# Performance work log

Hardware: AMD Instinct MI355X
Metric: run time of the kernel (lower is better)

The kernel has to match this reference:

```python
import jax, jax.numpy as jnp
import numpy as np

L_IN, L_FREQ, L_OUT = 128, 64, 64
C_IN, C_OUT, T_DIM = 64, 64, 256
SPIN = 1

# ---------- self-contained spin-weighted SHT (MW sampling), replacing s2fft ----------

def _mw_thetas(L, extended):
    n = 2 * L - 1 if extended else L
    return (2 * np.arange(n) + 1) * np.pi / (2 * L - 1)

def _wigner_d_stack(L, thetas, n):
    # d^l_{m,n}(theta) = <l,m| exp(-i theta Jy) |l,n>, computed via eigh of the
    # Hermitian angular-momentum operator Jy. Output (ntheta, L, 2L-1), m at col L-1+m.
    nth = len(thetas)
    out = np.zeros((nth, L, 2 * L - 1), dtype=np.float64)
    for l in range(abs(n), L):
        dim = 2 * l + 1
        m = np.arange(-l, l).astype(np.float64)
        ap = np.sqrt(l * (l + 1.0) - m * (m + 1.0))
        Jy = np.zeros((dim, dim), dtype=np.complex128)
        i = np.arange(dim - 1)
        Jy[i + 1, i] = -0.5j * ap
        Jy[i, i + 1] = 0.5j * ap
        lam, V = np.linalg.eigh(Jy)
        coeff = V * np.conj(V[l + n, :])[None, :]
        phases = np.exp(-1j * np.outer(lam, thetas))
        out[:, l, L - 1 - l:L + l] = (coeff @ phases).T.real
    return out

def _mw_quad_weights(L):
    # per-theta weights on the mirror-extended grid: q_t = (1/(2L-1)) sum_k w(k) e^{ik theta_t}
    # with w(k) = int_0^pi e^{ik t} sin(t) dt
    k = np.arange(-(L - 1), L)
    den = np.where(np.abs(k) == 1, 1, 1 - k * k).astype(np.float64)
    w = np.where(k % 2 == 0, 2.0 / den, 0.0).astype(np.complex128)
    w[k == 1] = 0.5j * np.pi
    w[k == -1] = -0.5j * np.pi
    th = _mw_thetas(L, True)
    return ((w[None, :] * np.exp(1j * np.outer(th, k))).sum(1) / (2 * L - 1)).real

# transform kernels are constants (built once at import, numpy)
_D_FWD = jnp.asarray(_wigner_d_stack(L_IN, _mw_thetas(L_IN, True), -SPIN) * _mw_quad_weights(L_IN)[:, None, None], jnp.float32)
_D_INV = jnp.asarray(_wigner_d_stack(L_OUT, _mw_thetas(L_OUT, False), -SPIN), jnp.float32)
_CL_IN = jnp.asarray(((-1.0) ** SPIN) * np.sqrt((2 * np.arange(L_IN) + 1) / (4 * np.pi)), jnp.float32)
_CL_OUT = jnp.asarray(((-1.0) ** SPIN) * np.sqrt((2 * np.arange(L_OUT) + 1) / (4 * np.pi)), jnp.float32)
_m_all = np.arange(-(L_IN - 1), L_IN)
_PARITY = jnp.asarray(np.where((_m_all + SPIN) % 2 == 0, 1.0, -1.0), jnp.float32)

def sht_forward(x):
    # x: (L_IN, 2*L_IN-1, C) real spatial -> flm: (L_IN, 2*L_IN-1, C) complex, m at L_IN-1+m
    nphi = 2 * L_IN - 1
    ftm = jnp.fft.fftshift(jnp.fft.fft(x, axis=1), axes=1) * (2 * jnp.pi / nphi)
    # mirror extension in theta with (-1)^(m+spin) parity (all channels at once)
    g_ext = jnp.concatenate([ftm, _PARITY[None, :, None] * ftm[::-1][1:]], axis=0)
    flm = jnp.einsum('tlm,tmc->lmc', _D_FWD, g_ext)
    return flm * _CL_IN[:, None, None]

def sht_inverse(flm):
    # flm: (L_OUT, 2*L_OUT-1, C) complex -> (L_OUT, 2*L_OUT-1, C) real spatial
    ftm = jnp.einsum('tlm,lmc->tmc', _D_INV, flm * _CL_OUT[:, None, None])
    return (jnp.fft.ifft(jnp.fft.ifftshift(ftm, axes=1), axis=1) * (2 * L_OUT - 1)).real

def resize_flm(flm, l_in, l_out):
    # centered truncation / zero-pad of (L, 2L-1, C) harmonic coefficients
    if l_out <= l_in:
        d = l_in - l_out
        return flm[:l_out, d:d + 2 * l_out - 1]
    d = l_out - l_in
    return jnp.pad(flm, ((0, d), (d, d), (0, 0)))

# ---------- inputs and parameters ----------

def setup_inputs():
    key = jax.random.key(0)
    ks = jax.random.split(key, 12)
    n = lambda i, shape, s: jax.random.normal(ks[i], shape, jnp.float32) * s
    return {
        'x': jax.random.normal(ks[0], (L_IN, 2 * L_IN - 1, C_IN), jnp.float32),
        't_emb': jax.random.normal(ks[1], (T_DIM,), jnp.float32),
        'spec_conv_w': n(2, (C_IN, C_OUT), (1.0 / C_IN) ** 0.5),
        'spec_conv_b': jnp.zeros((C_OUT,), jnp.float32),
        'spec_wr': n(3, (L_FREQ, C_IN, C_OUT), (0.5 / C_IN) ** 0.5),
        'spec_wi': n(4, (L_FREQ, C_IN, C_OUT), (0.5 / C_IN) ** 0.5),
        'spec_tr_w': n(5, (T_DIM, L_FREQ), (1.0 / T_DIM) ** 0.5),
        'spec_tr_b': jnp.zeros((L_FREQ,), jnp.float32),
        'spec_ti_w': n(6, (T_DIM, L_FREQ), (1.0 / T_DIM) ** 0.5),
        'spec_ti_b': jnp.zeros((L_FREQ,), jnp.float32),
        'spat_conv1_w': n(7, (C_IN, C_OUT), (1.0 / C_IN) ** 0.5),
        'spat_conv1_b': jnp.zeros((C_OUT,), jnp.float32),
        'spat_t_w': n(8, (T_DIM, 2 * C_OUT), (1.0 / T_DIM) ** 0.5),
        'spat_t_b': jnp.zeros((2 * C_OUT,), jnp.float32),
        'spat_weight': n(9, (C_OUT, C_OUT), 0.01),
        'spat_conv2_w': n(10, (C_OUT, C_OUT), (1.0 / C_OUT) ** 0.5),
        'spat_conv2_b': jnp.zeros((C_OUT,), jnp.float32),
        'ln_scale': jnp.ones((C_OUT,), jnp.float32),
        'ln_bias': jnp.zeros((C_OUT,), jnp.float32),
    }

def reference(x, t_emb, spec_conv_w, spec_conv_b, spec_wr, spec_wi, spec_tr_w, spec_tr_b, spec_ti_w, spec_ti_b, spat_conv1_w, spat_conv1_b, spat_t_w, spat_t_b, spat_weight, spat_conv2_w, spat_conv2_b, ln_scale, ln_bias):
    # ----- SphericalSpectralTimeConv branch -----
    flm = sht_forward(x)                                   # (L_IN, 2L_IN-1, C_IN) complex
    flm = resize_flm(flm, L_IN, L_FREQ)                    # (L_FREQ, 2L_FREQ-1, C_IN)
    conv_flm = jnp.einsum('lmi,io->lmo', flm, spec_conv_w) + spec_conv_b
    t_c = (t_emb @ spec_tr_w + spec_tr_b) + 1j * (t_emb @ spec_ti_w + spec_ti_b)   # (L_FREQ,)
    w = t_c[:, None, None] * (spec_wr + 1j * spec_wi)      # (L_FREQ, C_IN, C_OUT)
    flm = jnp.einsum('lmi,lio->lmo', flm, w) + conv_flm
    xs = sht_inverse(resize_flm(flm, L_FREQ, L_OUT))       # (L_OUT, 2L_OUT-1, C_OUT) real
    xs = xs / (jnp.linalg.norm(xs, axis=-1, keepdims=True) + 1e-6)
    # ----- SpatialTimeConv branch (path='down') -----
    h = jnp.einsum('lmi,io->lmo', x, spat_conv1_w) + spat_conv1_b
    t = t_emb @ spat_t_w + spat_t_b
    w_t, b_t = t[:C_OUT], t[C_OUT:]
    h = jnp.einsum('lmi,io->lmo', h, w_t[None, :] * spat_weight)
    h = sht_inverse(resize_flm(sht_forward(h), L_IN, L_OUT))
    h = jnp.einsum('lmi,io->lmo', h, spat_conv2_w) + spat_conv2_b + b_t
    # ----- combine: add, gelu, LayerNorm (eps=1e-6 over channels) -----
    y = jax.nn.gelu(xs + h)
    mu = jnp.mean(y, axis=-1, keepdims=True)
    var = jnp.var(y, axis=-1, keepdims=True)
    return (y - mu) * jax.lax.rsqrt(var + 1e-6) * ln_scale + ln_bias
```

## Files before the change

### kernel.cpp

```cpp
#include <hip/hip_runtime.h>
#include <math.h>

#define DPI 3.141592653589793238462643383279502884

__device__ __forceinline__ float wave_sum64(float v) {
#pragma unroll
  for (int off = 32; off > 0; off >>= 1) v += __shfl_xor(v, off, 64);
  return v;
}

__device__ __forceinline__ float gelu_tanh(float v) {
  float u = 0.7978845608028654f * (v + 0.044715f * v * v * v);
  return 0.5f * v * (1.0f + tanhf(u));
}

#define CN255F ((float)(-2.0 * DPI / 255.0))
#define CN127F ((float)(2.0 * DPI / 127.0))

__global__ __launch_bounds__(256) void ct_setup(
    float* __restrict__ Deff, float* __restrict__ Dinv,
    const float* __restrict__ temb, const float* __restrict__ trw,
    const float* __restrict__ trb, const float* __restrict__ tiw,
    const float* __restrict__ tib, const float* __restrict__ stw,
    const float* __restrict__ stb, const float* __restrict__ scw,
    const float* __restrict__ swr, const float* __restrict__ swi,
    const float* __restrict__ c1w, const float* __restrict__ c1b,
    const float* __restrict__ sweight,
    float2* __restrict__ A2, float* __restrict__ Mm,
    float* __restrict__ bias2, float* __restrict__ tv) {
  __shared__ double red[64];
  __shared__ float clf[64];
  __shared__ float fb1[256];
  __shared__ float fb2[256];
  int b = blockIdx.x;
  int tid = threadIdx.x;
  if (b >= 255) {
    if (b < 319) {
      int l = b - 255;
      fb1[tid] = temb[tid] * trw[tid * 64 + l];
      fb2[tid] = temb[tid] * tiw[tid * 64 + l];
      __syncthreads();
      for (int s = 128; s > 0; s >>= 1) {
        if (tid < s) { fb1[tid] += fb1[tid + s]; fb2[tid] += fb2[tid + s]; }
        __syncthreads();
      }
      float tr = fb1[0] + trb[l], ti = fb2[0] + tib[l];
      int o = tid & 63, iq = tid >> 6;
      for (int i = iq * 16; i < iq * 16 + 16; ++i) {
        int idx = (l * 64 + i) * 64 + o;
        float r = swr[idx], s2 = swi[idx];
        A2[idx] = make_float2(scw[i * 64 + o] + tr * r - ti * s2, tr * s2 + ti * r);
      }
    } else if (b < 383) {
      int j = b - 319;
      int o = tid & 63, part = tid >> 6;
      float p = 0.f;
      for (int k = part * 64; k < part * 64 + 64; ++k)
        p = fmaf(temb[k], stw[k * 128 + o], p);
      fb1[part * 64 + o] = p;
      __syncthreads();
      if (part == 0) fb2[o] = fb1[o] + fb1[64 + o] + fb1[128 + o] + fb1[192 + o] + stb[o];
      __syncthreads();
      float tvo = fb2[o];
      float q = 0.f;
      for (int i = part * 16; i < part * 16 + 16; ++i)
        q = fmaf(c1w[j * 64 + i], sweight[i * 64 + o], q);
      __syncthreads();
      fb1[part * 64 + o] = q;
      __syncthreads();
      if (part == 0) Mm[j * 64 + o] = tvo * (fb1[o] + fb1[64 + o] + fb1[128 + o] + fb1[192 + o]);
      if (j == 0) {
        float bq = 0.f;
        for (int i = part * 16; i < part * 16 + 16; ++i)
          bq = fmaf(c1b[i], sweight[i * 64 + o], bq);
        __syncthreads();
        fb1[part * 64 + o] = bq;
        __syncthreads();
        if (part == 0) bias2[o] = tvo * (fb1[o] + fb1[64 + o] + fb1[128 + o] + fb1[192 + o]);
      }
    } else {
      int o = tid & 127, part = tid >> 7;
      float p = 0.f;
      for (int k = part * 128; k < part * 128 + 128; ++k)
        p = fmaf(temb[k], stw[k * 128 + o], p);
      fb1[part * 128 + o] = p;
      __syncthreads();
      if (part == 0) tv[o] = fb1[o] + fb1[128 + o] + stb[o];
    }
    return;
  }
  int mode = (b < 128) ? 0 : 1;
  if (tid < 64) clf[tid] = (float)(-sqrt((2.0 * tid + 1.0) / (4.0 * DPI)));
  int t, mm;
  if (mode == 0) { t = b; mm = tid; }
  else { mm = b - 128; t = tid; }
  double denomN = (mode == 0) ? 255.0 : 127.0;
  double beta = (2.0 * t + 1.0) * DPI / denomN;
  float coeff;
  if (mode == 0) {
    if (tid < 63) {
      int k = 2 * (tid + 1);
      red[tid] = 8.0 * cos((double)k * beta) / (1.0 - (double)k * (double)k);
    } else if (tid == 63) {
      red[63] = 4.0;
    }
    __syncthreads();
    for (int s = 32; s > 0; s >>= 1) {
      if (tid < s) red[tid] += red[tid + s];
      __syncthreads();
    }
    double s = red[0] / 255.0;
    if (t == 127) s *= 0.5;
    coeff = (float)(s * (2.0 * DPI / 255.0));
    if (tid >= 127) return;
  } else {
    __syncthreads();
    coeff = 1.0f;
    if (tid >= 64) return;
  }
  int m = mm - 63;
  double cb = cos(beta);
  double ch = cos(0.5 * beta), sh = sin(0.5 * beta);
  int am = (m < 0) ? -m : m;
  int l0v = (am > 1) ? am : 1;
  double seed;
  if (m >= 1) {
    double j = (double)m;
    double K = exp(0.5 * (lgamma(2.0 * j + 1.0) - lgamma(j) - lgamma(j + 2.0)));
    double sgn = ((m + 1) & 1) ? -1.0 : 1.0;
    seed = sgn * K * pow(ch, j - 1.0) * pow(sh, j + 1.0);
  } else if (m <= -1) {
    double j = (double)(-m);
    double K = exp(0.5 * (lgamma(2.0 * j + 1.0) - lgamma(j) - lgamma(j + 2.0)));
    seed = K * pow(ch, j + 1.0) * pow(sh, j - 1.0);
  } else {
    seed = -sqrt(2.0) * sh * ch;
  }
  float dl = (float)seed, dm1 = 0.0f, S_cur = 0.0f;
  float cbf = (float)cb, mf = (float)m;
  for (int l = 0; l < 64; ++l) {
    float val = 0.0f;
    if (l >= l0v) {
      val = dl * coeff * clf[l];
      float Ld = (float)l, lp = Ld + 1.0f;
      float S_next = sqrtf((lp * lp - mf * mf) * (lp * lp - 1.0f));
      float num1 = (2.0f * Ld + 1.0f) * (Ld * lp * cbf + mf);
      float dn = (num1 * dl - lp * S_cur * dm1) / (Ld * S_next);
      dm1 = dl; dl = dn; S_cur = S_next;
    }
    if (mode == 0) Deff[((size_t)t * 127 + mm) * 64 + l] = val;
    else Dinv[((size_t)mm * 64 + l) * 64 + t] = val;
  }
}

__global__ __launch_bounds__(256) void ct_dft(const float* __restrict__ x,
                                              float* __restrict__ Are, float* __restrict__ Aim,
                                              float* __restrict__ Bre, float* __restrict__ Bim) {
  __shared__ float xs_[64][64];
  __shared__ float tsr[64][64], tsi[64][64];
  int t = blockIdx.x, mh = blockIdx.y, ph = blockIdx.z;
  float* ore = ph ? Bre : Are;
  float* oim = ph ? Bim : Aim;
  int pbase = ph * 128;
  int Ktot = ph ? 127 : 128;
  int tid = threadIdx.x;
  int cg_ = tid & 15, mg = tid >> 4;
  float accr[4][4], acci[4][4];
#pragma unroll
  for (int j = 0; j < 4; ++j)
#pragma unroll
    for (int q = 0; q < 4; ++q) { accr[j][q] = 0.f; acci[j][q] = 0.f; }
  for (int k0 = 0; k0 < Ktot; k0 += 64) {
    int kn = (Ktot - k0 < 64) ? Ktot - k0 : 64;
    __syncthreads();
    {
      int r = tid >> 2, c4 = (tid & 3) * 16;
      if (r < kn) {
        const float4* src = (const float4*)(x + ((size_t)t * 255 + pbase + k0 + r) * 64 + c4);
        float4* dst = (float4*)&xs_[r][c4];
        dst[0] = src[0]; dst[1] = src[1]; dst[2] = src[2]; dst[3] = src[3];
      }
    }
    for (int e = tid; e < 64 * 64; e += 256) {
      int r = e >> 6, mi = e & 63;
      if (r < kn) {
        int gcol = mh * 64 + mi; if (gcol > 126) gcol = 126;
        int p = pbase + k0 + r;
        float ang = CN255F * (float)((gcol - 63) * p);
        float sv, cv;
        __sincosf(ang, &sv, &cv);
        tsr[r][mi] = cv; tsi[r][mi] = sv;
      }
    }
    __syncthreads();
#pragma unroll 4
    for (int k = 0; k < kn; ++k) {
      float4 xv = *(const float4*)&xs_[k][cg_ * 4];
      float4 tr4 = *(const float4*)&tsr[k][mg * 4];
      float4 ti4 = *(const float4*)&tsi[k][mg * 4];
      float xv4[4] = {xv.x, xv.y, xv.z, xv.w};
      float trv[4] = {tr4.x, tr4.y, tr4.z, tr4.w};
      float tiv[4] = {ti4.x, ti4.y, ti4.z, ti4.w};
#pragma unroll
      for (int j = 0; j < 4; ++j)
#pragma unroll
        for (int q = 0; q < 4; ++q) {
          accr[j][q] = fmaf(xv4[q], trv[j], accr[j][q]);
          acci[j][q] = fmaf(xv4[q], tiv[j], acci[j][q]);
        }
    }
  }
#pragma unroll
  for (int j = 0; j < 4; ++j) {
    int gmm = mh * 64 + mg * 4 + j;
    if (gmm > 126) continue;
    size_t ob = ((size_t)t * 127 + gmm) * 64 + cg_ * 4;
    *(float4*)(ore + ob) = make_float4(accr[j][0], accr[j][1], accr[j][2], accr[j][3]);
    *(float4*)(oim + ob) = make_float4(acci[j][0], acci[j][1], acci[j][2], acci[j][3]);
  }
}

__global__ __launch_bounds__(256) void ct_projf(const float* __restrict__ Deff,
                                                const float* __restrict__ fAre,
                                                const float* __restrict__ fAim,
                                                const float* __restrict__ fBre,
                                                const float* __restrict__ fBim,
                                                float* __restrict__ flmA_re, float* __restrict__ flmA_im,
                                                float* __restrict__ flmB_re, float* __restrict__ flmB_im) {
  __shared__ float Dsh[64][32];
  __shared__ float fr_[64][64], fi_[64][64];
  int mm = blockIdx.x, lh = blockIdx.y, th = blockIdx.z;
  float* ore = th ? flmB_re : flmA_re;
  float* oim = th ? flmB_im : flmA_im;
  int tb = th * 64;
  int tid = threadIdx.x;
  int cg_ = tid & 15, lg = tid >> 4;
  for (int e = tid; e < 64 * 32; e += 256) {
    int r = e >> 5, li = e & 31;
    Dsh[r][li] = Deff[((size_t)(tb + r) * 127 + mm) * 64 + lh * 32 + li];
  }
  for (int e = tid; e < 64 * 64; e += 256) {
    int r = e >> 6, c = e & 63;
    size_t idx = ((size_t)(tb + r) * 127 + mm) * 64 + c;
    fr_[r][c] = fAre[idx] + fBre[idx];
    fi_[r][c] = fAim[idx] + fBim[idx];
  }
  __syncthreads();
  float ar[2][4], ai[2][4];
#pragma unroll
  for (int li = 0; li < 2; ++li)
#pragma unroll
    for (int q = 0; q < 4; ++q) { ar[li][q] = 0.f; ai[li][q] = 0.f; }
#pragma unroll 4
  for (int k = 0; k < 64; ++k) {
    float4 fr4 = *(const float4*)&fr_[k][cg_ * 4];
    float4 fi4 = *(const float4*)&fi_[k][cg_ * 4];
    float2 d2 = *(const float2*)&Dsh[k][lg * 2];
    float frv[4] = {fr4.x, fr4.y, fr4.z, fr4.w};
    float fiv[4] = {fi4.x, fi4.y, fi4.z, fi4.w};
    float dv[2] = {d2.x, d2.y};
#pragma unroll
    for (int li = 0; li < 2; ++li)
#pragma unroll
      for (int q = 0; q < 4; ++q) {
        ar[li][q] = fmaf(dv[li], frv[q], ar[li][q]);
        ai[li][q] = fmaf(dv[li], fiv[q], ai[li][q]);
      }
  }
#pragma unroll
  for (int li = 0; li < 2; ++li) {
    size_t row = ((size_t)mm * 64 + lh * 32 + lg * 2 + li) * 64 + cg_ * 4;
    *(float4*)(ore + row) = make_float4(ar[li][0], ar[li][1], ar[li][2], ar[li][3]);
    *(float4*)(oim + row) = make_float4(ai[li][0], ai[li][1], ai[li][2], ai[li][3]);
  }
}

__global__ __launch_bounds__(256) void ct_mix(const float* __restrict__ flmA_re,
                                              const float* __restrict__ flmA_im,
                                              const float* __restrict__ flmB_re,
                                              const float* __restrict__ flmB_im,
                                              const float2* __restrict__ A2,
                                              const float* __restrict__ Mm,
                                              const float* __restrict__ scb,
                                              const float* __restrict__ bias2,
                                              const float* __restrict__ Deff,
                                              float* __restrict__ s_re, float* __restrict__ s_im,
                                              float* __restrict__ h_re, float* __restrict__ h_im) {
  __shared__ float Ar_[64][32], Ai_[64][32], Msh[64][32];
  __shared__ float Br_[64][65], Bi_[64][65];
  __shared__ float rb[256];
  int l = blockIdx.x, mh = blockIdx.y, oh = blockIdx.z;
  int tid = threadIdx.x;
  int og = tid & 15, mg = tid >> 4;
  rb[tid] = (mh == 0 && tid < 128) ? Deff[((size_t)tid * 127 + 63) * 64 + l] : 0.f;
  __syncthreads();
  for (int s = 128; s > 0; s >>= 1) {
    if (tid < s) rb[tid] += rb[tid + s];
    __syncthreads();
  }
  float slv = rb[0];
  for (int e = tid; e < 64 * 32; e += 256) {
    int r = e >> 5, oi = e & 31;
    float2 aa = A2[((size_t)l * 64 + r) * 64 + oh * 32 + oi];
    Ar_[r][oi] = aa.x; Ai_[r][oi] = aa.y;
    Msh[r][oi] = Mm[r * 64 + oh * 32 + oi];
  }
  for (int e = tid; e < 64 * 64; e += 256) {
    int mi = e >> 6, i = e & 63;
    int gmm = mh * 64 + mi; if (gmm > 126) gmm = 126;
    size_t idx = ((size_t)gmm * 64 + l) * 64 + i;
    Br_[mi][i] = flmA_re[idx] + flmB_re[idx];
    Bi_[mi][i] = flmA_im[idx] + flmB_im[idx];
  }
  __syncthreads();
  int o0 = oh * 32 + og * 2;
  float b0[2] = {scb[o0], scb[o0 + 1]};
  float sr[4][2], si[4][2], hr[4][2], hi[4][2];
#pragma unroll
  for (int jm = 0; jm < 4; ++jm)
#pragma unroll
    for (int qo = 0; qo < 2; ++qo) {
      sr[jm][qo] = b0[qo]; si[jm][qo] = 0.f; hr[jm][qo] = 0.f; hi[jm][qo] = 0.f;
    }
#pragma unroll 4
  for (int k = 0; k < 64; ++k) {
    float2 ar2 = *(const float2*)&Ar_[k][og * 2];
    float2 ai2 = *(const float2*)&Ai_[k][og * 2];
    float2 mv2 = *(const float2*)&Msh[k][og * 2];
    float br4[4], bi4[4];
#pragma unroll
    for (int jm = 0; jm < 4; ++jm) {
      br4[jm] = Br_[mg * 4 + jm][k];
      bi4[jm] = Bi_[mg * 4 + jm][k];
    }
    float arv[2] = {ar2.x, ar2.y}, aiv[2] = {ai2.x, ai2.y}, mvv[2] = {mv2.x, mv2.y};
#pragma unroll
    for (int jm = 0; jm < 4; ++jm)
#pragma unroll
      for (int qo = 0; qo < 2; ++qo) {
        sr[jm][qo] = fmaf(br4[jm], arv[qo], sr[jm][qo]);
        sr[jm][qo] = fmaf(-bi4[jm], aiv[qo], sr[jm][qo]);
        si[jm][qo] = fmaf(br4[jm], aiv[qo], si[jm][qo]);
        si[jm][qo] = fmaf(bi4[jm], arv[qo], si[jm][qo]);
        hr[jm][qo] = fmaf(br4[jm], mvv[qo], hr[jm][qo]);
        hi[jm][qo] = fmaf(bi4[jm], mvv[qo], hi[jm][qo]);
      }
  }
  float bb[2] = {bias2[o0], bias2[o0 + 1]};
#pragma unroll
  for (int jm = 0; jm < 4; ++jm) {
    int gmm = mh * 64 + mg * 4 + jm;
    if (gmm > 126) continue;
    if (gmm == 63) {
#pragma unroll
      for (int qo = 0; qo < 2; ++qo)
        hr[jm][qo] = fmaf(255.0f * slv, bb[qo], hr[jm][qo]);
    }
    size_t row = ((size_t)gmm * 64 + l) * 64 + o0;
    *(float2*)(s_re + row) = make_float2(sr[jm][0], sr[jm][1]);
    *(float2*)(s_im + row) = make_float2(si[jm][0], si[jm][1]);
    *(float2*)(h_re + row) = make_float2(hr[jm][0], hr[jm][1]);
    *(float2*)(h_im + row) = make_float2(hi[jm][0], hi[jm][1]);
  }
}

__global__ __launch_bounds__(256) void ct_proji(const float* __restrict__ Dinv,
                                                const float* __restrict__ s_re,
                                                const float* __restrict__ s_im,
                                                const float* __restrict__ h_re,
                                                const float* __restrict__ h_im,
                                                float* __restrict__ fos_re, float* __restrict__ fos_im,
                                                float* __restrict__ foh_re, float* __restrict__ foh_im) {
  __shared__ float Dsh[64][64];
  __shared__ float Br_[64][32], Bi_[64][32];
  int mm = blockIdx.x, br = blockIdx.y, ch = blockIdx.z;
  const float* ire = br ? h_re : s_re;
  const float* iim = br ? h_im : s_im;
  float* ore = br ? foh_re : fos_re;
  float* oim = br ? foh_im : fos_im;
  int tid = threadIdx.x;
  int cg_ = tid & 15, tg = tid >> 4;
  for (int e = tid; e < 64 * 64; e += 256) {
    int r = e >> 6, tt = e & 63;
    Dsh[r][tt] = Dinv[((size_t)mm * 64 + r) * 64 + tt];
  }
  for (int e = tid; e < 64 * 32; e += 256) {
    int r = e >> 5, cc = e & 31;
    size_t idx = ((size_t)mm * 64 + r) * 64 + ch * 32 + cc;
    Br_[r][cc] = ire[idx];
    Bi_[r][cc] = iim[idx];
  }
  __syncthreads();
  float ar[4][2], ai[4][2];
#pragma unroll
  for (int j = 0; j < 4; ++j)
#pragma unroll
    for (int q = 0; q < 2; ++q) { ar[j][q] = 0.f; ai[j][q] = 0.f; }
#pragma unroll 4
  for (int k = 0; k < 64; ++k) {
    float4 d4 = *(const float4*)&Dsh[k][tg * 4];
    float2 fr2 = *(const float2*)&Br_[k][cg_ * 2];
    float2 fi2 = *(const float2*)&Bi_[k][cg_ * 2];
    float dv[4] = {d4.x, d4.y, d4.z, d4.w};
    float frv[2] = {fr2.x, fr2.y}, fiv[2] = {fi2.x, fi2.y};
#pragma unroll
    for (int j = 0; j < 4; ++j)
#pragma unroll
      for (int q = 0; q < 2; ++q) {
        ar[j][q] = fmaf(dv[j], frv[q], ar[j][q]);
        ai[j][q] = fmaf(dv[j], fiv[q], ai[j][q]);
      }
  }
#pragma unroll
  for (int j = 0; j < 4; ++j) {
    int t = tg * 4 + j;
    size_t ob = ((size_t)t * 127 + mm) * 64 + ch * 32 + cg_ * 2;
    *(float2*)(ore + ob) = make_float2(ar[j][0], ar[j][1]);
    *(float2*)(oim + ob) = make_float2(ai[j][0], ai[j][1]);
  }
}

__global__ __launch_bounds__(256) void ct_idft(const float* __restrict__ fos_re,
                                               const float* __restrict__ fos_im,
                                               const float* __restrict__ foh_re,
                                               const float* __restrict__ foh_im,
                                               float* __restrict__ xsbA, float* __restrict__ xsbB,
                                               float* __restrict__ hsbA, float* __restrict__ hsbB) {
  __shared__ float Ar_[32][64], Ai_[32][64], Br_[32][64], Bi_[32][64];
  int t = blockIdx.x, br = blockIdx.y;
  int z = blockIdx.z;
  int ph = z >> 1, kh = z & 1;
  const float* fre = br ? foh_re : fos_re;
  const float* fim = br ? foh_im : fos_im;
  float* outp = br ? (kh ? hsbB : hsbA) : (kh ? xsbB : xsbA);
  int kbase = kh * 64;
  int Ktot = kh ? 63 : 64;
  int tid = threadIdx.x;
  int cg_ = tid & 15, pg = tid >> 4;
  float acc[4][4];
#pragma unroll
  for (int j = 0; j < 4; ++j)
#pragma unroll
    for (int q = 0; q < 4; ++q) acc[j][q] = 0.f;
  for (int k0 = 0; k0 < Ktot; k0 += 32) {
    int kn = (Ktot - k0 < 32) ? Ktot - k0 : 32;
    __syncthreads();
    for (int e = tid; e < 32 * 64; e += 256) {
      int r = e >> 6, j = e & 63;
      if (r < kn) {
        int gmm = kbase + k0 + r;
        int gp = ph * 64 + j; if (gp > 126) gp = 126;
        float ang = CN127F * (float)((gmm - 63) * gp);
        float sv, cv;
        __sincosf(ang, &sv, &cv);
        Ar_[r][j] = cv; Ai_[r][j] = sv;
        size_t bidx = ((size_t)t * 127 + gmm) * 64 + j;
        Br_[r][j] = fre[bidx]; Bi_[r][j] = fim[bidx];
      }
    }
    __syncthreads();
#pragma unroll 4
    for (int k = 0; k < kn; ++k) {
      float4 a_r = *(const float4*)&Ar_[k][pg * 4];
      float4 a_i = *(const float4*)&Ai_[k][pg * 4];
      float4 b_r = *(const float4*)&Br_[k][cg_ * 4];
      float4 b_i = *(const float4*)&Bi_[k][cg_ * 4];
      float arv[4] = {a_r.x, a_r.y, a_r.z, a_r.w};
      float aiv[4] = {a_i.x, a_i.y, a_i.z, a_i.w};
      float brv[4] = {b_r.x, b_r.y, b_r.z, b_r.w};
      float biv[4] = {b_i.x, b_i.y, b_i.z, b_i.w};
#pragma unroll
      for (int j = 0; j < 4; ++j)
#pragma unroll
        for (int q = 0; q < 4; ++q) {
          acc[j][q] = fmaf(brv[q], arv[j], acc[j][q]);
          acc[j][q] = fmaf(biv[q], -aiv[j], acc[j][q]);
        }
    }
  }
#pragma unroll
  for (int j = 0; j < 4; ++j) {
    int gp = ph * 64 + pg * 4 + j;
    if (gp > 126) continue;
    *(float4*)(outp + ((size_t)t * 127 + gp) * 64 + cg_ * 4) =
        make_float4(acc[j][0], acc[j][1], acc[j][2], acc[j][3]);
  }
}

__global__ __launch_bounds__(256) void ct_fin(const float* __restrict__ xsbA,
                                              const float* __restrict__ xsbB,
                                              const float* __restrict__ hsbA,
                                              const float* __restrict__ hsbB,
                                              const float* __restrict__ c2w,
                                              const float* __restrict__ c2b,
                                              const float* __restrict__ tv,
                                              const float* __restrict__ lns,
                                              const float* __restrict__ lnb,
                                              float* __restrict__ out) {
  int w = threadIdx.x >> 6, lane = threadIdx.x & 63;
  size_t row = (size_t)blockIdx.x * 4 + w;
  size_t base = row * 64 + lane;
  float hv = hsbA[base] + hsbB[base];
  float xv = xsbA[base] + xsbB[base];
  float acc = c2b[lane] + tv[64 + lane];
#pragma unroll 16
  for (int i = 0; i < 64; ++i)
    acc = fmaf(__shfl(hv, i, 64), c2w[i * 64 + lane], acc);
  float ss = wave_sum64(xv * xv);
  xv = xv / (sqrtf(ss) + 1e-6f);
  float y = xv + acc;
  float g = gelu_tanh(y);
  float mu = wave_sum64(g) * (1.0f / 64.0f);
  float d = g - mu;
  float var = wave_sum64(d * d) * (1.0f / 64.0f);
  out[base] = d * rsqrtf(var + 1e-6f) * lns[lane] + lnb[lane];
}

extern "C" void kernel_launch(void* const* d_in, const int* in_sizes, int n_in,
                              void* d_out, int out_size, void* d_ws, size_t ws_size,
                              hipStream_t stream) {
  const float* x = (const float*)d_in[0];
  const float* temb = (const float*)d_in[1];
  const float* scw = (const float*)d_in[2];
  const float* scb = (const float*)d_in[3];
  const float* swr = (const float*)d_in[4];
  const float* swi = (const float*)d_in[5];
  const float* strw = (const float*)d_in[6];
  const float* strb = (const float*)d_in[7];
  const float* stiw = (const float*)d_in[8];
  const float* stib = (const float*)d_in[9];
  const float* c1w = (const float*)d_in[10];
  const float* c1b = (const float*)d_in[11];
  const float* stw = (const float*)d_in[12];
  const float* stb = (const float*)d_in[13];
  const float* sweight = (const float*)d_in[14];
  const float* c2w = (const float*)d_in[15];
  const float* c2b = (const float*)d_in[16];
  const float* lns = (const float*)d_in[17];
  const float* lnb = (const float*)d_in[18];
  float* out = (float*)d_out;

  char* base = (char*)d_ws;
  size_t off = 0;
  auto alloc = [&](size_t bytes) -> void* {
    void* p = base + off;
    off += (bytes + 255) & ~(size_t)255;
    return p;
  };
  float* tv = (float*)alloc(128 * sizeof(float));
  float* Mm = (float*)alloc(4096 * sizeof(float));
  float* bias2 = (float*)alloc(64 * sizeof(float));
  float2* A2 = (float2*)alloc(262144 * sizeof(float2));
  float* Deff = (float*)alloc(1040384 * sizeof(float));
  float* Dinv = (float*)alloc(520192 * sizeof(float));
  float* ftmA_re = (float*)alloc(1040384 * sizeof(float));
  float* ftmA_im = (float*)alloc(1040384 * sizeof(float));
  float* ftmB_re = (float*)alloc(1040384 * sizeof(float));
  float* ftmB_im = (float*)alloc(1040384 * sizeof(float));
  float* flmA_re = (float*)alloc(520192 * sizeof(float));
  float* flmA_im = (float*)alloc(520192 * sizeof(float));
  float* flmB_re = (float*)alloc(520192 * sizeof(float));
  float* flmB_im = (float*)alloc(520192 * sizeof(float));
  if (off > ws_size) return;
  float* s_re = ftmA_re;
  float* s_im = ftmA_im;
  float* h_re = ftmB_re;
  float* h_im = ftmB_im;
  float* fos_re = Deff;
  float* fos_im = Deff + 520192;
  float* foh_re = flmA_re;
  float* foh_im = flmA_im;
  float* xsbA = flmB_re;
  float* xsbB = flmB_im;
  float* hsbA = ftmA_re;
  float* hsbB = ftmA_im;

  hipLaunchKernelGGL(ct_setup, dim3(384), dim3(256), 0, stream, Deff, Dinv,
                     temb, strw, strb, stiw, stib, stw, stb,
                     scw, swr, swi, c1w, c1b, sweight, A2, Mm, bias2, tv);
  hipLaunchKernelGGL(ct_dft, dim3(128, 2, 2), dim3(256), 0, stream, x,
                     ftmA_re, ftmA_im, ftmB_re, ftmB_im);
  hipLaunchKernelGGL(ct_projf, dim3(127, 2, 2), dim3(256), 0, stream, Deff,
                     ftmA_re, ftmA_im, ftmB_re, ftmB_im,
                     flmA_re, flmA_im, flmB_re, flmB_im);
  hipLaunchKernelGGL(ct_mix, dim3(64, 2, 2), dim3(256), 0, stream,
                     flmA_re, flmA_im, flmB_re, flmB_im, A2, Mm, scb, bias2, Deff,
                     s_re, s_im, h_re, h_im);
  hipLaunchKernelGGL(ct_proji, dim3(127, 2, 2), dim3(256), 0, stream, Dinv,
                     s_re, s_im, h_re, h_im, fos_re, fos_im, foh_re, foh_im);
  hipLaunchKernelGGL(ct_idft, dim3(64, 2, 4), dim3(256), 0, stream,
                     fos_re, fos_im, foh_re, foh_im, xsbA, xsbB, hsbA, hsbB);
  hipLaunchKernelGGL(ct_fin, dim3(2032), dim3(256), 0, stream, xsbA, xsbB, hsbA, hsbB,
                     c2w, c2b, tv, lns, lnb, out);
}
```

Measured before the change: 211.9 us.

## Merge setup and DFT kernels into one launch, use float log-factorial seeds

Combines the former setup kernel (Wigner tables, time-embedding weights) and the DFT kernel into one heterogeneous kernel that dispatches on block index, so the independent work runs concurrently in a single launch. The Wigner seed computation swaps double-precision lgamma/pow for a float prefix-sum log-factorial table and __expf. Sharing one 48KB shared-memory buffer across roles may lower occupancy for the small setup blocks, and the float seeds add precision risk for large |m|.

```diff
diff --git a/kernel.cpp b/kernel.cpp
--- a/kernel.cpp
+++ b/kernel.cpp
@@ -17,86 +17,96 @@
 #define CN255F ((float)(-2.0 * DPI / 255.0))
 #define CN127F ((float)(2.0 * DPI / 127.0))
 
-__global__ __launch_bounds__(256) void ct_setup(
-    float* __restrict__ Deff, float* __restrict__ Dinv,
-    const float* __restrict__ temb, const float* __restrict__ trw,
-    const float* __restrict__ trb, const float* __restrict__ tiw,
-    const float* __restrict__ tib, const float* __restrict__ stw,
-    const float* __restrict__ stb, const float* __restrict__ scw,
-    const float* __restrict__ swr, const float* __restrict__ swi,
-    const float* __restrict__ c1w, const float* __restrict__ c1b,
-    const float* __restrict__ sweight,
-    float2* __restrict__ A2, float* __restrict__ Mm,
-    float* __restrict__ bias2, float* __restrict__ tv) {
-  __shared__ double red[64];
-  __shared__ float clf[64];
-  __shared__ float fb1[256];
-  __shared__ float fb2[256];
-  int b = blockIdx.x;
-  int tid = threadIdx.x;
-  if (b >= 255) {
-    if (b < 319) {
-      int l = b - 255;
-      fb1[tid] = temb[tid] * trw[tid * 64 + l];
-      fb2[tid] = temb[tid] * tiw[tid * 64 + l];
-      __syncthreads();
-      for (int s = 128; s > 0; s >>= 1) {
-        if (tid < s) { fb1[tid] += fb1[tid + s]; fb2[tid] += fb2[tid + s]; }
-        __syncthreads();
+
+__device__ __forceinline__ void dft_block(int idx, int tid, const float* __restrict__ x,
+                                          float* __restrict__ Are, float* __restrict__ Aim,
+                                          float* __restrict__ Bre, float* __restrict__ Bim,
+                                          char* sm) {
+  float* xs_ = (float*)sm;
+  float* tsr = (float*)(sm + 16384);
+  float* tsi = (float*)(sm + 32768);
+  int t = idx >> 2, mh = (idx >> 1) & 1, ph = idx & 1;
+  float* ore = ph ? Bre : Are;
+  float* oim = ph ? Bim : Aim;
+  int pbase = ph * 128;
+  int Ktot = ph ? 127 : 128;
+  int cg_ = tid & 15, mg = tid >> 4;
+  float accr[4][4], acci[4][4];
+#pragma unroll
+  for (int j = 0; j < 4; ++j)
+#pragma unroll
+    for (int q = 0; q < 4; ++q) { accr[j][q] = 0.f; acci[j][q] = 0.f; }
+  for (int k0 = 0; k0 < Ktot; k0 += 64) {
+    int kn = (Ktot - k0 < 64) ? Ktot - k0 : 64;
+    __syncthreads();
+    {
+      int r = tid >> 2, c4 = (tid & 3) * 16;
+      if (r < kn) {
+        const float4* src = (const float4*)(x + ((size_t)t * 255 + pbase + k0 + r) * 64 + c4);
+        float4* dst = (float4*)&xs_[r * 64 + c4];
+        dst[0] = src[0]; dst[1] = src[1]; dst[2] = src[2]; dst[3] = src[3];
       }
-      float tr = fb1[0] + trb[l], ti = fb2[0] + tib[l];
-      int o = tid & 63, iq = tid >> 6;
-      for (int i = iq * 16; i < iq * 16 + 16; ++i) {
-        int idx = (l * 64 + i) * 64 + o;
-        float r = swr[idx], s2 = swi[idx];
-        A2[idx] = make_float2(scw[i * 64 + o] + tr * r - ti * s2, tr * s2 + ti * r);
+    }
+    for (int e = tid; e < 64 * 64; e += 256) {
+      int r = e >> 6, mi = e & 63;
+      if (r < kn) {
+        int gcol = mh * 64 + mi; if (gcol > 126) gcol = 126;
+        int p = pbase + k0 + r;
+        float ang = CN255F * (float)((gcol - 63) * p);
+        float sv, cv;
+        __sincosf(ang, &sv, &cv);
+        tsr[r * 64 + mi] = cv; tsi[r * 64 + mi] = sv;
       }
-    } else if (b < 383) {
-      int j = b - 319;
-      int o = tid & 63, part = tid >> 6;
-      float p = 0.f;
-      for (int k = part * 64; k < part * 64 + 64; ++k)
-        p = fmaf(temb[k], stw[k * 128 + o], p);
-      fb1[part * 64 + o] = p;
-      __syncthreads();
-      if (part == 0) fb2[o] = fb1[o] + fb1[64 + o] + fb1[128 + o] + fb1[192 + o] + stb[o];
-      __syncthreads();
-      float tvo = fb2[o];
-      float q = 0.f;
-      for (int i = part * 16; i < part * 16 + 16; ++i)
-        q = fmaf(c1w[j * 64 + i], sweight[i * 64 + o], q);
-      __syncthreads();
-      fb1[part * 64 + o] = q;
-      __syncthreads();
-      if (part == 0) Mm[j * 64 + o] = tvo * (fb1[o] + fb1[64 + o] + fb1[128 + o] + fb1[192 + o]);
-      if (j == 0) {
-        float bq = 0.f;
-        for (int i = part * 16; i < part * 16 + 16; ++i)
-          bq = fmaf(c1b[i], sweight[i * 64 + o], bq);
-        __syncthreads();
-        fb1[part * 64 + o] = bq;
-        __syncthreads();
-        if (part == 0) bias2[o] = tvo * (fb1[o] + fb1[64 + o] + fb1[128 + o] + fb1[192 + o]);
-      }
-    } else {
-      int o = tid & 127, part = tid >> 7;
-      float p = 0.f;
-      for (int k = part * 128; k < part * 128 + 128; ++k)
-        p = fmaf(temb[k], stw[k * 128 + o], p);
-      fb1[part * 128 + o] = p;
-      __syncthreads();
-      if (part == 0) tv[o] = fb1[o] + fb1[128 + o] + stb[o];
-    }
-    return;
-  }
-  int mode = (b < 128) ? 0 : 1;
+    }
+    __syncthreads();
+#pragma unroll 4
+    for (int k = 0; k < kn; ++k) {
+      float4 xv = *(const float4*)&xs_[k * 64 + cg_ * 4];
+      float4 tr4 = *(const float4*)&tsr[k * 64 + mg * 4];
+      float4 ti4 = *(const float4*)&tsi[k * 64 + mg * 4];
+      float xv4[4] = {xv.x, xv.y, xv.z, xv.w};
+      float trv[4] = {tr4.x, tr4.y, tr4.z, tr4.w};
+      float tiv[4] = {ti4.x, ti4.y, ti4.z, ti4.w};
+#pragma unroll
+      for (int j = 0; j < 4; ++j)
+#pragma unroll
+        for (int q = 0; q < 4; ++q) {
+          accr[j][q] = fmaf(xv4[q], trv[j], accr[j][q]);
+          acci[j][q] = fmaf(xv4[q], tiv[j], acci[j][q]);
+        }
+    }
+  }
+#pragma unroll
+  for (int j = 0; j < 4; ++j) {
+    int gmm = mh * 64 + mg * 4 + j;
+    if (gmm > 126) continue;
+    size_t ob = ((size_t)t * 127 + gmm) * 64 + cg_ * 4;
+    *(float4*)(ore + ob) = make_float4(accr[j][0], accr[j][1], accr[j][2], accr[j][3]);
+    *(float4*)(oim + ob) = make_float4(acci[j][0], acci[j][1], acci[j][2], acci[j][3]);
+  }
+}
+
+__device__ __forceinline__ void wigner_block(int wb, int tid, float* __restrict__ Deff,
+                                             float* __restrict__ Dinv, char* sm) {
+  float* LF = (float*)sm;
+  double* red = (double*)(sm + 512);
+  float* clf = (float*)(sm + 1024);
+  int mode = (wb < 128) ? 0 : 1;
+  int t, mm;
+  if (mode == 0) { t = wb; mm = tid; }
+  else { mm = wb - 128; t = (tid < 64) ? tid : 63; }
   if (tid < 64) clf[tid] = (float)(-sqrt((2.0 * tid + 1.0) / (4.0 * DPI)));
-  int t, mm;
-  if (mode == 0) { t = b; mm = tid; }
-  else { mm = b - 128; t = tid; }
+  if (tid < 128) LF[tid] = (tid == 0) ? 0.f : logf((float)tid);
+  __syncthreads();
+  for (int s = 1; s < 128; s <<= 1) {
+    float add = (tid < 128 && tid >= s) ? LF[tid - s] : 0.f;
+    __syncthreads();
+    if (tid < 128) LF[tid] += add;
+    __syncthreads();
+  }
   double denomN = (mode == 0) ? 255.0 : 127.0;
   double beta = (2.0 * t + 1.0) * DPI / denomN;
-  float coeff;
+  float coeff = 1.0f;
   if (mode == 0) {
     if (tid < 63) {
       int k = 2 * (tid + 1);
@@ -112,32 +122,30 @@
     double s = red[0] / 255.0;
     if (t == 127) s *= 0.5;
     coeff = (float)(s * (2.0 * DPI / 255.0));
-    if (tid >= 127) return;
-  } else {
-    __syncthreads();
-    coeff = 1.0f;
-    if (tid >= 64) return;
-  }
+  }
+  bool active = (mode == 0) ? (tid < 127) : (tid < 64);
+  if (!active) return;
   int m = mm - 63;
-  double cb = cos(beta);
-  double ch = cos(0.5 * beta), sh = sin(0.5 * beta);
+  double chd, shd;
+  sincos(0.5 * beta, &shd, &chd);
+  float cbf = (float)cos(beta);
+  float chf = (float)chd, shf = (float)shd;
   int am = (m < 0) ? -m : m;
   int l0v = (am > 1) ? am : 1;
-  double seed;
-  if (m >= 1) {
-    double j = (double)m;
-    double K = exp(0.5 * (lgamma(2.0 * j + 1.0) - lgamma(j) - lgamma(j + 2.0)));
-    double sgn = ((m + 1) & 1) ? -1.0 : 1.0;
-    seed = sgn * K * pow(ch, j - 1.0) * pow(sh, j + 1.0);
-  } else if (m <= -1) {
-    double j = (double)(-m);
-    double K = exp(0.5 * (lgamma(2.0 * j + 1.0) - lgamma(j) - lgamma(j + 2.0)));
-    seed = K * pow(ch, j + 1.0) * pow(sh, j - 1.0);
+  float seed;
+  if (m == 0) {
+    seed = -1.4142135623730951f * shf * chf;
   } else {
-    seed = -sqrt(2.0) * sh * ch;
-  }
-  float dl = (float)seed, dm1 = 0.0f, S_cur = 0.0f;
-  float cbf = (float)cb, mf = (float)m;
+    int j = am;
+    float lch = logf(chf), lsh = logf(shf);
+    float e0 = 0.5f * (LF[2 * j] - LF[j - 1] - LF[j + 1]);
+    float expo = (m >= 1) ? e0 + (float)(j - 1) * lch + (float)(j + 1) * lsh
+                          : e0 + (float)(j + 1) * lch + (float)(j - 1) * lsh;
+    float sv = __expf(expo);
+    seed = (m >= 1 && ((m + 1) & 1)) ? -sv : sv;
+  }
+  float dl = seed, dm1 = 0.0f, S_cur = 0.0f;
+  float mf = (float)m;
   for (int l = 0; l < 64; ++l) {
     float val = 0.0f;
     if (l >= l0v) {
@@ -153,71 +161,98 @@
   }
 }
 
-__global__ __launch_bounds__(256) void ct_dft(const float* __restrict__ x,
-                                              float* __restrict__ Are, float* __restrict__ Aim,
-                                              float* __restrict__ Bre, float* __restrict__ Bim) {
-  __shared__ float xs_[64][64];
-  __shared__ float tsr[64][64], tsi[64][64];
-  int t = blockIdx.x, mh = blockIdx.y, ph = blockIdx.z;
-  float* ore = ph ? Bre : Are;
-  float* oim = ph ? Bim : Aim;
-  int pbase = ph * 128;
-  int Ktot = ph ? 127 : 128;
+__device__ __forceinline__ void a2_block(int l, int tid, const float* __restrict__ temb,
+                                         const float* __restrict__ trw, const float* __restrict__ trb,
+                                         const float* __restrict__ tiw, const float* __restrict__ tib,
+                                         const float* __restrict__ scw, const float* __restrict__ swr,
+                                         const float* __restrict__ swi, float2* __restrict__ A2,
+                                         char* sm) {
+  float* fb1 = (float*)sm;
+  float* fb2 = (float*)(sm + 1024);
+  fb1[tid] = temb[tid] * trw[tid * 64 + l];
+  fb2[tid] = temb[tid] * tiw[tid * 64 + l];
+  __syncthreads();
+  for (int s = 128; s > 0; s >>= 1) {
+    if (tid < s) { fb1[tid] += fb1[tid + s]; fb2[tid] += fb2[tid + s]; }
+    __syncthreads();
+  }
+  float tr = fb1[0] + trb[l], ti = fb2[0] + tib[l];
+  int o = tid & 63, iq = tid >> 6;
+  for (int i = iq * 16; i < iq * 16 + 16; ++i) {
+    int idx = (l * 64 + i) * 64 + o;
+    float r = swr[idx], s2 = swi[idx];
+    A2[idx] = make_float2(scw[i * 64 + o] + tr * r - ti * s2, tr * s2 + ti * r);
+  }
+}
+
+__device__ __forceinline__ void m_block(int j, int tid, const float* __restrict__ temb,
+                                        const float* __restrict__ stw, const float* __restrict__ stb,
+                                        const float* __restrict__ c1w, const float* __restrict__ c1b,
+                                        const float* __restrict__ sweight, float* __restrict__ Mm,
+                                        float* __restrict__ bias2, char* sm) {
+  float* fb1 = (float*)sm;
+  float* fb2 = (float*)(sm + 1024);
+  int o = tid & 63, part = tid >> 6;
+  float p = 0.f;
+  for (int k = part * 64; k < part * 64 + 64; ++k)
+    p = fmaf(temb[k], stw[k * 128 + o], p);
+  fb1[part * 64 + o] = p;
+  __syncthreads();
+  if (part == 0) fb2[o] = fb1[o] + fb1[64 + o] + fb1[128 + o] + fb1[192 + o] + stb[o];
+  __syncthreads();
+  float tvo = fb2[o];
+  float q = 0.f;
+  for (int i = part * 16; i < part * 16 + 16; ++i)
+    q = fmaf(c1w[j * 64 + i], sweight[i * 64 + o], q);
+  __syncthreads();
+  fb1[part * 64 + o] = q;
+  __syncthreads();
+  if (part == 0) Mm[j * 64 + o] = tvo * (fb1[o] + fb1[64 + o] + fb1[128 + o] + fb1[192 + o]);
+  if (j == 0) {
+    float bq = 0.f;
+    for (int i = part * 16; i < part * 16 + 16; ++i)
+      bq = fmaf(c1b[i], sweight[i * 64 + o], bq);
+    __syncthreads();
+    fb1[part * 64 + o] = bq;
+    __syncthreads();
+    if (part == 0) bias2[o] = tvo * (fb1[o] + fb1[64 + o] + fb1[128 + o] + fb1[192 + o]);
+  }
+}
+
+__device__ __forceinline__ void tv_block(int tid, const float* __restrict__ temb,
+                                         const float* __restrict__ stw, const float* __restrict__ stb,
+                                         float* __restrict__ tv, char* sm) {
+  float* fb1 = (float*)sm;
+  int o = tid & 127, part = tid >> 7;
+  float p = 0.f;
+  for (int k = part * 128; k < part * 128 + 128; ++k)
+    p = fmaf(temb[k], stw[k * 128 + o], p);
+  fb1[part * 128 + o] = p;
+  __syncthreads();
+  if (part == 0) tv[o] = fb1[o] + fb1[128 + o] + stb[o];
+}
+
+__global__ __launch_bounds__(256) void ct_pre(
+    const float* __restrict__ x, const float* __restrict__ temb,
+    const float* __restrict__ trw, const float* __restrict__ trb,
+    const float* __restrict__ tiw, const float* __restrict__ tib,
+    const float* __restrict__ stw, const float* __restrict__ stb,
+    const float* __restrict__ scw, const float* __restrict__ swr,
+    const float* __restrict__ swi, const float* __restrict__ c1w,
+    const float* __restrict__ c1b, const float* __restrict__ sweight,
+    float* __restrict__ Deff, float* __restrict__ Dinv,
+    float2* __restrict__ A2, float* __restrict__ Mm,
+    float* __restrict__ bias2, float* __restrict__ tv,
+    float* __restrict__ ftmA_re, float* __restrict__ ftmA_im,
+    float* __restrict__ ftmB_re, float* __restrict__ ftmB_im) {
+  __shared__ __align__(16) char sm[49152];
+  int vb = blockIdx.x;
   int tid = threadIdx.x;
-  int cg_ = tid & 15, mg = tid >> 4;
-  float accr[4][4], acci[4][4];
-#pragma unroll
-  for (int j = 0; j < 4; ++j)
-#pragma unroll
-    for (int q = 0; q < 4; ++q) { accr[j][q] = 0.f; acci[j][q] = 0.f; }
-  for (int k0 = 0; k0 < Ktot; k0 += 64) {
-    int kn = (Ktot - k0 < 64) ? Ktot - k0 : 64;
-    __syncthreads();
-    {
-      int r = tid >> 2, c4 = (tid & 3) * 16;
-      if (r < kn) {
-        const float4* src = (const float4*)(x + ((size_t)t * 255 + pbase + k0 + r) * 64 + c4);
-        float4* dst = (float4*)&xs_[r][c4];
-        dst[0] = src[0]; dst[1] = src[1]; dst[2] = src[2]; dst[3] = src[3];
-      }
-    }
-    for (int e = tid; e < 64 * 64; e += 256) {
-      int r = e >> 6, mi = e & 63;
-      if (r < kn) {
-        int gcol = mh * 64 + mi; if (gcol > 126) gcol = 126;
-        int p = pbase + k0 + r;
-        float ang = CN255F * (float)((gcol - 63) * p);
-        float sv, cv;
-        __sincosf(ang, &sv, &cv);
-        tsr[r][mi] = cv; tsi[r][mi] = sv;
-      }
-    }
-    __syncthreads();
-#pragma unroll 4
-    for (int k = 0; k < kn; ++k) {
-      float4 xv = *(const float4*)&xs_[k][cg_ * 4];
-      float4 tr4 = *(const float4*)&tsr[k][mg * 4];
-      float4 ti4 = *(const float4*)&tsi[k][mg * 4];
-      float xv4[4] = {xv.x, xv.y, xv.z, xv.w};
-      float trv[4] = {tr4.x, tr4.y, tr4.z, tr4.w};
-      float tiv[4] = {ti4.x, ti4.y, ti4.z, ti4.w};
-#pragma unroll
-      for (int j = 0; j < 4; ++j)
-#pragma unroll
-        for (int q = 0; q < 4; ++q) {
-          accr[j][q] = fmaf(xv4[q], trv[j], accr[j][q]);
-          acci[j][q] = fmaf(xv4[q], tiv[j], acci[j][q]);
-        }
-    }
-  }
-#pragma unroll
-  for (int j = 0; j < 4; ++j) {
-    int gmm = mh * 64 + mg * 4 + j;
-    if (gmm > 126) continue;
-    size_t ob = ((size_t)t * 127 + gmm) * 64 + cg_ * 4;
-    *(float4*)(ore + ob) = make_float4(accr[j][0], accr[j][1], accr[j][2], accr[j][3]);
-    *(float4*)(oim + ob) = make_float4(acci[j][0], acci[j][1], acci[j][2], acci[j][3]);
-  }
+  if (vb < 512) dft_block(vb, tid, x, ftmA_re, ftmA_im, ftmB_re, ftmB_im, sm);
+  else if (vb < 767) wigner_block(vb - 512, tid, Deff, Dinv, sm);
+  else if (vb < 831) a2_block(vb - 767, tid, temb, trw, trb, tiw, tib, scw, swr, swi, A2, sm);
+  else if (vb < 895) m_block(vb - 831, tid, temb, stw, stb, c1w, c1b, sweight, Mm, bias2, sm);
+  else tv_block(tid, temb, stw, stb, tv, sm);
 }
 
 __global__ __launch_bounds__(256) void ct_projf(const float* __restrict__ Deff,
@@ -575,10 +610,10 @@
   float* hsbA = ftmA_re;
   float* hsbB = ftmA_im;
 
-  hipLaunchKernelGGL(ct_setup, dim3(384), dim3(256), 0, stream, Deff, Dinv,
-                     temb, strw, strb, stiw, stib, stw, stb,
-                     scw, swr, swi, c1w, c1b, sweight, A2, Mm, bias2, tv);
-  hipLaunchKernelGGL(ct_dft, dim3(128, 2, 2), dim3(256), 0, stream, x,
+  hipLaunchKernelGGL(ct_pre, dim3(896), dim3(256), 0, stream,
+                     x, temb, strw, strb, stiw, stib, stw, stb,
+                     scw, swr, swi, c1w, c1b, sweight,
+                     Deff, Dinv, A2, Mm, bias2, tv,
                      ftmA_re, ftmA_im, ftmB_re, ftmB_im);
   hipLaunchKernelGGL(ct_projf, dim3(127, 2, 2), dim3(256), 0, stream, Deff,
                      ftmA_re, ftmA_im, ftmB_re, ftmB_im,
```

Measured after the change: 202.9 us. 4.3% less time.
